# Optimization experiments

Measured on AMD Instinct MI355X. Metric: run time of the kernel, lower is better.

Reference implementation:

```python
import jax, jax.numpy as jnp
from jax import lax
import numpy as np

# Dims: batch, input channels (=3*C), output channels, kernel size, spatial
B, CIN, C, K, H, W = 8, 576, 192, 3, 56, 56
KK = K * K  # number of kernel positions


def setup_inputs() -> dict:
    key = jax.random.key(0)
    k1, k2, k3, k4 = jax.random.split(key, 4)
    x = jax.random.normal(k1, (B, CIN, H, W), jnp.float32)
    # 1x1 conv producing per-channel, per-position dynamic logits (C*KK outputs)
    fc_w = jax.random.normal(k2, (C * KK, CIN), jnp.float32) * 0.05
    # per-position grouped conv kernels: (KK, C_out, CIN//C=3, K, K)
    w1 = jax.random.normal(k3, (KK, C, CIN // C, K, K), jnp.float32) * 0.1
    # per-position depthwise conv kernels: (KK, C, K, K)
    w2 = jax.random.normal(k4, (KK, C, K, K), jnp.float32) * 0.1
    return {"x": x, "fc_w": fc_w, "w1": w1, "w2": w2}


def reference(x, fc_w, w1, w2):
    b = x.shape[0]
    # dynamic softmax weights over the KK kernel positions: (b, C, KK, H, W)
    logits = jnp.einsum('oc,bchw->bohw', fc_w, x).reshape(b, C, KK, H, W)
    attn = jax.nn.softmax(logits, axis=2)

    # dep_conv1: per-position grouped conv (3C -> C, groups=C), vmapped over KK
    def conv1(wi):  # wi: (C, 3, K, K)
        return lax.conv_general_dilated(x, wi, (1, 1), 'SAME',
                                        feature_group_count=C)

    feat = jax.nn.relu(jax.vmap(conv1)(w1))  # (KK, b, C, H, W)

    # dep_conv2: per-position depthwise conv (C -> C, groups=C)
    def conv2(fi, wi):  # fi: (b, C, H, W), wi: (C, K, K)
        return lax.conv_general_dilated(fi, wi[:, None], (1, 1), 'SAME',
                                        feature_group_count=C)

    out_pos = jax.vmap(conv2)(feat, w2)  # (KK, b, C, H, W)

    # softmax-weighted aggregation over kernel positions
    out = jnp.einsum('ibchw,bcihw->bchw', out_pos, attn)  # (b, C, H, W)
    return out
```

## Files before the change

kernel.cpp:

```cpp
#include <hip/hip_runtime.h>
#include <hip/hip_bf16.h>

constexpr int Bn   = 8;
constexpr int Cin  = 576;
constexpr int Cc   = 192;
constexpr int Hh   = 56;
constexpr int Ww   = 56;
constexpr int HWn  = Hh * Ww;
constexpr int CKK  = Cc * 9;

constexpr int GM = 1792;
constexpr int GK = 576;
constexpr int GN = Bn * HWn;
constexpr int NKSTEP = GK / 32;

using f16x8 = __attribute__((ext_vector_type(8))) _Float16;
using f32x4 = __attribute__((ext_vector_type(4))) float;

__device__ __forceinline__ void async_copy16(void* lds, const void* gptr) {
    __builtin_amdgcn_global_load_lds(
        (const __attribute__((address_space(1))) unsigned int*)gptr,
        (__attribute__((address_space(3))) unsigned int*)lds, 16, 0, 0);
}

__device__ __forceinline__ float blo(unsigned int u) { return __uint_as_float(u << 16); }
__device__ __forceinline__ float bhi(unsigned int u) { return __uint_as_float(u & 0xffff0000u); }
__device__ __forceinline__ unsigned short bf16bits(float f) {
    union { __hip_bfloat16 h; unsigned short u; } c; c.h = __float2bfloat16(f); return c.u;
}

__global__ __launch_bounds__(256) void cast_fcw_kernel(
    const float* __restrict__ fcw, _Float16* __restrict__ out)
{
    int idx = blockIdx.x * 256 + threadIdx.x;
    int e = idx * 4;
    if (e >= GM * GK) return;
    int row = e / GK;
    union { ushort4 u; _Float16 h[4]; } pk;
    if (row < CKK) {
        float4 v = *(const float4*)&fcw[e];
        pk.h[0] = (_Float16)v.x; pk.h[1] = (_Float16)v.y;
        pk.h[2] = (_Float16)v.z; pk.h[3] = (_Float16)v.w;
    } else {
        pk.h[0] = pk.h[1] = pk.h[2] = pk.h[3] = (_Float16)0.f;
    }
    *(ushort4*)&out[e] = pk.u;
}

__global__ __launch_bounds__(256) void transpose_cast_kernel(
    const float* __restrict__ x, _Float16* __restrict__ xt)
{
    __shared__ float t[32][65];
    const int b = blockIdx.z, k0 = blockIdx.y * 32, hw0 = blockIdx.x * 64;
    const int tid = threadIdx.x;
    const int col = tid & 63, kr = tid >> 6;
#pragma unroll
    for (int p = 0; p < 8; p++) {
        int k = kr + p * 4;
        t[k][col] = x[(size_t)(b * Cin + k0 + k) * HWn + hw0 + col];
    }
    __syncthreads();
    const int row = tid >> 2, cq = (tid & 3) * 8;
    union { uint4 u; _Float16 h[8]; } pk;
#pragma unroll
    for (int j = 0; j < 8; j++) pk.h[j] = (_Float16)t[cq + j][row];
    *(uint4*)&xt[(size_t)(b * HWn + hw0 + row) * GK + k0 + cq] = pk.u;
}

__global__ __launch_bounds__(256, 2) void gemm_mfma_kernel(
    const _Float16* __restrict__ A, const _Float16* __restrict__ Bm,
    __hip_bfloat16* __restrict__ logits)
{
    const int lin = blockIdx.x;
    const int g = lin & 7, s = lin >> 3;
    const int mt = s % 7, nt = (s / 7) * 8 + g;
    if (nt >= 196) return;

    __shared__ _Float16 As[2][256 * 32];
    __shared__ _Float16 Bs[2][128 * 32];

    const int tid = threadIdx.x;
    const int n0 = nt * 128;
    const int m0 = mt * 256;
    const int lane = tid & 63;
    const int wave = tid >> 6;
    const int wm = (wave >> 1) * 128;
    const int wn = (wave & 1) * 64;
    const int lm = lane & 15;
    const int lc = lane >> 4;

    const int lrow = tid >> 2;
    const int koff = (((tid & 3) ^ ((tid >> 3) & 3)) << 3);

    int offA[8], offB[4];
#pragma unroll
    for (int i = 0; i < 8; i++) {
        int ra = wm + i * 16 + lm;
        offA[i] = ra * 32 + ((lc ^ ((ra >> 1) & 3)) << 3);
    }
#pragma unroll
    for (int j = 0; j < 4; j++) {
        int rb = wn + j * 16 + lm;
        offB[j] = rb * 32 + ((lc ^ ((rb >> 1) & 3)) << 3);
    }

    const _Float16* pA = A  + (size_t)(m0 + lrow) * GK + koff;
    const _Float16* pB = Bm + (size_t)(n0 + lrow) * GK + koff;

#define STAGE(buf, kk)                                                         \
    do {                                                                       \
        async_copy16(&As[buf][(size_t)tid * 8],        pA + (kk));             \
        async_copy16(&As[buf][2048  + (size_t)tid * 8], pA +  64 * GK + (kk)); \
        async_copy16(&As[buf][4096  + (size_t)tid * 8], pA + 128 * GK + (kk)); \
        async_copy16(&As[buf][6144  + (size_t)tid * 8], pA + 192 * GK + (kk)); \
        async_copy16(&Bs[buf][(size_t)tid * 8],        pB + (kk));             \
        async_copy16(&Bs[buf][2048  + (size_t)tid * 8], pB +  64 * GK + (kk)); \
    } while (0)

    STAGE(0, 0);
    STAGE(1, 32);
    asm volatile("s_waitcnt vmcnt(6)" ::: "memory");

    f32x4 acc[8][4] = {};

    for (int t = 0; t < NKSTEP; ++t) {
        const int cur = t & 1;
        __builtin_amdgcn_s_barrier();
        asm volatile("" ::: "memory");

        const _Float16* Ab = &As[cur][0];
        const _Float16* Bb = &Bs[cur][0];
        f16x8 bf[4];
#pragma unroll
        for (int j = 0; j < 4; j++) bf[j] = *(const f16x8*)&Bb[offB[j]];
#pragma unroll
        for (int i = 0; i < 8; i++) {
            f16x8 a = *(const f16x8*)&Ab[offA[i]];
#pragma unroll
            for (int j = 0; j < 4; j++)
                acc[i][j] = __builtin_amdgcn_mfma_f32_16x16x32_f16(bf[j], a, acc[i][j], 0, 0, 0);
        }

        asm volatile("" ::: "memory");
        __builtin_amdgcn_s_barrier();

        if (t + 2 < NKSTEP) {
            STAGE(cur, (t + 2) * 32);
            asm volatile("s_waitcnt vmcnt(6)" ::: "memory");
        } else {
            asm volatile("s_waitcnt vmcnt(0)" ::: "memory");
        }
    }
#undef STAGE

    const int mcol = m0 + wm + lm;
#pragma unroll
    for (int i = 0; i < 8; i++) {
        int m = mcol + i * 16;
        if (m >= CKK) continue;
#pragma unroll
        for (int j = 0; j < 4; j++) {
            int n = n0 + wn + j * 16 + lc * 4;
            int b = n / HWn, hw2 = n - b * HWn;
            uint2 pk;
            pk.x = (unsigned)bf16bits(acc[i][j][0]) | ((unsigned)bf16bits(acc[i][j][1]) << 16);
            pk.y = (unsigned)bf16bits(acc[i][j][2]) | ((unsigned)bf16bits(acc[i][j][3]) << 16);
            *(uint2*)&logits[((size_t)b * CKK + m) * HWn + hw2] = pk;
        }
    }
}

__global__ __launch_bounds__(256, 4) void conv_fused_kernel(
    const float* __restrict__ x, const float* __restrict__ w1,
    const __hip_bfloat16* __restrict__ logits,
    const float* __restrict__ w2, float* __restrict__ out)
{
    const int c = blockIdx.x, hb = blockIdx.y, b = blockIdx.z;
    const int tid = threadIdx.x;
    const int h0 = hb * 14;

    __shared__ float xt[3][18][59];
    __shared__ unsigned short ft[9][16][62];

    for (int idx = tid; idx < 756; idx += 256) {
        int d = idx / 252, rem = idx - d * 252;
        int r = rem / 14, g = rem - r * 14;
        int h = h0 - 2 + r;
        float4 v = {0.f, 0.f, 0.f, 0.f};
        if (h >= 0 && h < Hh)
            v = *(const float4*)&x[((size_t)(b * Cin + 3 * c + d) * Hh + h) * Ww + 4 * g];
        xt[d][r][1 + 4 * g + 0] = v.x;
        xt[d][r][1 + 4 * g + 1] = v.y;
        xt[d][r][1 + 4 * g + 2] = v.z;
        xt[d][r][1 + 4 * g + 3] = v.w;
    }
    for (int idx = tid; idx < 108; idx += 256) {
        int d = idx / 36, rem = idx - d * 36;
        int r = rem >> 1, col = (rem & 1) ? 57 : 0;
        xt[d][r][col] = 0.f;
    }
    for (int idx = tid; idx < 288; idx += 256) {
        int i = idx / 32, rem = idx - i * 32;
        int r = rem >> 1, side = rem & 1;
        *(unsigned int*)&ft[i][r][side ? 58 : 0] = 0u;
    }

    const bool p2 = tid < 196;
    const int row2 = tid / 14, seg2 = tid - row2 * 14;
    const int hw2 = (h0 + row2) * Ww + 4 * seg2;

    __syncthreads();

    if (tid < 224) {
        const int row = tid / 14, seg = tid - (tid / 14) * 14;
        const int w0 = 4 * seg;
        const int fh = h0 - 1 + row;
        const bool valid = (fh >= 0) && (fh < Hh);

        float acc[9][4] = {};

#pragma unroll 1
        for (int d = 0; d < 3; d++) {
            float win[3][6];
#pragma unroll
            for (int u = 0; u < 3; u++)
#pragma unroll
                for (int k = 0; k < 6; k++)
                    win[u][k] = xt[d][row + u][w0 + k];

            const float* wb = w1 + (size_t)c * 27 + d * 9;
#pragma unroll
            for (int i = 0; i < 9; i++) {
                const float* wp = wb + (size_t)i * Cc * 27;
                float wgt[9];
#pragma unroll
                for (int j = 0; j < 9; j++) wgt[j] = wp[j];
#pragma unroll
                for (int u = 0; u < 3; u++)
#pragma unroll
                    for (int v = 0; v < 3; v++) {
                        float wv = wgt[u * 3 + v];
#pragma unroll
                        for (int p = 0; p < 4; p++)
                            acc[i][p] += win[u][p + v] * wv;
                    }
            }
        }

#pragma unroll
        for (int i = 0; i < 9; i++) {
            unsigned pk0 = 0u, pk1 = 0u;
            if (valid) {
                pk0 = (unsigned)bf16bits(fmaxf(acc[i][0], 0.f)) |
                      ((unsigned)bf16bits(fmaxf(acc[i][1], 0.f)) << 16);
                pk1 = (unsigned)bf16bits(fmaxf(acc[i][2], 0.f)) |
                      ((unsigned)bf16bits(fmaxf(acc[i][3], 0.f)) << 16);
            }
            unsigned int* dst = (unsigned int*)&ft[i][row][2 + w0];
            dst[0] = pk0; dst[1] = pk1;
        }
    }

    uint2 lv[9];
    if (p2) {
        const __hip_bfloat16* lbase = logits + ((size_t)b * CKK + c * 9) * HWn + hw2;
#pragma unroll
        for (int i = 0; i < 9; i++) lv[i] = *(const uint2*)&lbase[(size_t)i * HWn];
    }
    __syncthreads();

    if (p2) {
        const int w0 = 4 * seg2;

        float lg[9][4];
#pragma unroll
        for (int i = 0; i < 9; i++) {
            lg[i][0] = blo(lv[i].x); lg[i][1] = bhi(lv[i].x);
            lg[i][2] = blo(lv[i].y); lg[i][3] = bhi(lv[i].y);
        }
#pragma unroll
        for (int p = 0; p < 4; p++) {
            float mx = lg[0][p];
#pragma unroll
            for (int i = 1; i < 9; i++) mx = fmaxf(mx, lg[i][p]);
            float sum = 0.f;
#pragma unroll
            for (int i = 0; i < 9; i++) { lg[i][p] = __expf(lg[i][p] - mx); sum += lg[i][p]; }
            float inv = __builtin_amdgcn_rcpf(sum);
#pragma unroll
            for (int i = 0; i < 9; i++) lg[i][p] *= inv;
        }

        float oacc[4] = {};
#pragma unroll
        for (int i = 0; i < 9; i++) {
            const float* wp = w2 + ((size_t)i * Cc + c) * 9;
            float wgt[9];
#pragma unroll
            for (int j = 0; j < 9; j++) wgt[j] = wp[j];
            float cacc[4] = {};
#pragma unroll
            for (int u = 0; u < 3; u++) {
                const unsigned short* fr = &ft[i][row2 + u][w0];
                unsigned a0 = *(const unsigned*)(fr);
                unsigned a1 = *(const unsigned*)(fr + 2);
                unsigned b0 = *(const unsigned*)(fr + 4);
                unsigned b1 = *(const unsigned*)(fr + 6);
                float wf[8];
                wf[1] = bhi(a0);
                wf[2] = blo(a1);  wf[3] = bhi(a1);
                wf[4] = blo(b0);  wf[5] = bhi(b0);
                wf[6] = blo(b1);
#pragma unroll
                for (int v = 0; v < 3; v++) {
                    float wv = wgt[u * 3 + v];
#pragma unroll
                    for (int p = 0; p < 4; p++)
                        cacc[p] += wf[p + v + 1] * wv;
                }
            }
#pragma unroll
            for (int p = 0; p < 4; p++) oacc[p] += cacc[p] * lg[i][p];
        }

        float4 o;
        o.x = oacc[0]; o.y = oacc[1]; o.z = oacc[2]; o.w = oacc[3];
        *(float4*)&out[((size_t)(b * Cc + c)) * HWn + hw2] = o;
    }
}

extern "C" void kernel_launch(void* const* d_in, const int* in_sizes, int n_in,
                              void* d_out, int out_size, void* d_ws, size_t ws_size,
                              hipStream_t stream)
{
    const float* x    = (const float*)d_in[0];
    const float* fc_w = (const float*)d_in[1];
    const float* w1   = (const float*)d_in[2];
    const float* w2   = (const float*)d_in[3];
    float* out = (float*)d_out;

    char* ws = (char*)d_ws;
    __hip_bfloat16* logits = (__hip_bfloat16*)ws;
    _Float16* xt    = (_Float16*)(ws + (size_t)Bn * CKK * HWn * 2);
    _Float16* fcw16 = (_Float16*)(ws + (size_t)Bn * CKK * HWn * 2 + (size_t)GN * GK * 2);

    cast_fcw_kernel<<<(GM * GK / 4 + 255) / 256, 256, 0, stream>>>(fc_w, fcw16);
    transpose_cast_kernel<<<dim3(HWn / 64, GK / 32, Bn), 256, 0, stream>>>(x, xt);
    gemm_mfma_kernel<<<8 * 25 * 7, 256, 0, stream>>>(fcw16, xt, logits);
    conv_fused_kernel<<<dim3(Cc, 4, Bn), 256, 0, stream>>>(x, w1, logits, w2, out);
}
```

Baseline: 252.4 us.

## Compute grouped conv1 stage with f16 MFMA instead of scalar FMAs

The first grouped-conv stage (27 inputs per channel times 9 kernel positions) is recast as a small matrix multiply. Each lane holds an f16 fragment of the per-position weights and gathers im2col inputs from the shared tile, then issues a 16x16x32 f16 MFMA per 16-pixel group. The goal is to replace many scalar FMAs and repeated global weight loads with matrix-core work. In exchange, inputs and weights are rounded to fp16, the ft buffer is fully zeroed, stores become scattered 16-bit LDS writes, and the padded MFMA lanes waste work.

```diff
diff --git a/kernel.cpp b/kernel.cpp
--- a/kernel.cpp
+++ b/kernel.cpp
@@ -182,6 +182,32 @@
     __shared__ float xt[3][18][59];
     __shared__ unsigned short ft[9][16][62];
 
+    const int ln  = tid & 63;
+    const int wv  = tid >> 6;
+    const int px15 = ln & 15;
+    const int kc   = ln >> 4;
+
+    f16x8 wfr;
+    {
+        union { f16x8 v; _Float16 h[8]; } u;
+        const int pos = ln & 15;
+#pragma unroll
+        for (int j = 0; j < 8; j++) {
+            int k = kc * 8 + j;
+            float w = (pos < 9 && k < 27) ? w1[((size_t)pos * Cc + c) * 27 + k] : 0.f;
+            u.h[j] = (_Float16)w;
+        }
+        wfr = u.v;
+    }
+    int pre[8];
+#pragma unroll
+    for (int j = 0; j < 8; j++) {
+        int k = kc * 8 + j;
+        int kk = (k < 27) ? k : 0;
+        int d = kk / 9, r9 = kk - d * 9, uu = r9 / 3, vv = r9 - uu * 3;
+        pre[j] = d * (18 * 59) + uu * 59 + vv;
+    }
+
     for (int idx = tid; idx < 756; idx += 256) {
         int d = idx / 252, rem = idx - d * 252;
         int r = rem / 14, g = rem - r * 14;
@@ -199,10 +225,9 @@
         int r = rem >> 1, col = (rem & 1) ? 57 : 0;
         xt[d][r][col] = 0.f;
     }
-    for (int idx = tid; idx < 288; idx += 256) {
-        int i = idx / 32, rem = idx - i * 32;
-        int r = rem >> 1, side = rem & 1;
-        *(unsigned int*)&ft[i][r][side ? 58 : 0] = 0u;
+    {
+        unsigned int* ftu = (unsigned int*)&ft[0][0][0];
+        for (int idx = tid; idx < 4464; idx += 256) ftu[idx] = 0u;
     }
 
     const bool p2 = tid < 196;
@@ -211,53 +236,32 @@
 
     __syncthreads();
 
-    if (tid < 224) {
-        const int row = tid / 14, seg = tid - (tid / 14) * 14;
-        const int w0 = 4 * seg;
-        const int fh = h0 - 1 + row;
-        const bool valid = (fh >= 0) && (fh < Hh);
-
-        float acc[9][4] = {};
-
+    {
+        const float* xtf = &xt[0][0][0];
 #pragma unroll 1
-        for (int d = 0; d < 3; d++) {
-            float win[3][6];
-#pragma unroll
-            for (int u = 0; u < 3; u++)
-#pragma unroll
-                for (int k = 0; k < 6; k++)
-                    win[u][k] = xt[d][row + u][w0 + k];
-
-            const float* wb = w1 + (size_t)c * 27 + d * 9;
-#pragma unroll
-            for (int i = 0; i < 9; i++) {
-                const float* wp = wb + (size_t)i * Cc * 27;
-                float wgt[9];
-#pragma unroll
-                for (int j = 0; j < 9; j++) wgt[j] = wp[j];
-#pragma unroll
-                for (int u = 0; u < 3; u++)
-#pragma unroll
-                    for (int v = 0; v < 3; v++) {
-                        float wv = wgt[u * 3 + v];
-#pragma unroll
-                        for (int p = 0; p < 4; p++)
-                            acc[i][p] += win[u][p + v] * wv;
+        for (int rr = 0; rr < 4; rr++) {
+            const int row = wv * 4 + rr;
+            const int fh = h0 - 1 + row;
+            const bool rowvalid = (fh >= 0) && (fh < Hh);
+#pragma unroll
+            for (int g = 0; g < 4; g++) {
+                const int fw = g * 16 + px15;
+                const int rb = row * 59 + fw;
+                union { f16x8 v; _Float16 h[8]; } bu;
+#pragma unroll
+                for (int j = 0; j < 8; j++)
+                    bu.h[j] = (_Float16)xtf[pre[j] + rb];
+                f32x4 d0 = {0.f, 0.f, 0.f, 0.f};
+                d0 = __builtin_amdgcn_mfma_f32_16x16x32_f16(wfr, bu.v, d0, 0, 0, 0);
+                if (rowvalid && fw < Ww) {
+#pragma unroll
+                    for (int r = 0; r < 4; r++) {
+                        int pos = kc * 4 + r;
+                        if (pos < 9)
+                            ft[pos][row][2 + fw] = bf16bits(fmaxf(d0[r], 0.f));
                     }
+                }
             }
-        }
-
-#pragma unroll
-        for (int i = 0; i < 9; i++) {
-            unsigned pk0 = 0u, pk1 = 0u;
-            if (valid) {
-                pk0 = (unsigned)bf16bits(fmaxf(acc[i][0], 0.f)) |
-                      ((unsigned)bf16bits(fmaxf(acc[i][1], 0.f)) << 16);
-                pk1 = (unsigned)bf16bits(fmaxf(acc[i][2], 0.f)) |
-                      ((unsigned)bf16bits(fmaxf(acc[i][3], 0.f)) << 16);
-            }
-            unsigned int* dst = (unsigned int*)&ft[i][row][2 + w0];
-            dst[0] = pk0; dst[1] = pk1;
         }
     }
 
@@ -313,10 +317,10 @@
                 wf[6] = blo(b1);
 #pragma unroll
                 for (int v = 0; v < 3; v++) {
-                    float wv = wgt[u * 3 + v];
+                    float wv2 = wgt[u * 3 + v];
 #pragma unroll
                     for (int p = 0; p < 4; p++)
-                        cacc[p] += wf[p + v + 1] * wv;
+                        cacc[p] += wf[p + v + 1] * wv2;
                 }
             }
 #pragma unroll
```

Result: slower. 258.4 us (+2.4%).
